# Kernel tuning notes

Measured on AMD Instinct MI355X. Metric: run time of the kernel, lower is better.

Reference implementation:

```python
import jax, jax.numpy as jnp
import numpy as np

N_NODES = 100000   # embedding table rows
FEAT = 512         # feat_dim F
BATCH = 8192       # seed nodes per batch
DEG = 32           # sampled neighbors per node (col 0 = self)
BN_EPS = 1e-5


def setup_inputs() -> dict:
    key = jax.random.key(0)
    ks = jax.random.split(key, 6)
    feat_table = jax.random.normal(ks[0], (N_NODES, FEAT), dtype=jnp.float32)
    W_gen = jax.random.normal(ks[1], (2 * FEAT, 2 * FEAT), dtype=jnp.float32) * 0.02
    weight1 = jax.random.normal(ks[2], (3 * FEAT, 3 * FEAT), dtype=jnp.float32) * 0.02
    gamma = jnp.ones((3 * FEAT,), dtype=jnp.float32)
    beta = jnp.zeros((3 * FEAT,), dtype=jnp.float32)
    nodes = jax.random.randint(ks[3], (BATCH,), 0, N_NODES, dtype=jnp.int32)
    neigh_idx = jax.random.randint(ks[4], (BATCH, DEG), 0, N_NODES, dtype=jnp.int32)
    neigh_idx = neigh_idx.at[:, 0].set(nodes)  # self node included, as in samp_neighs
    return {"feat_table": feat_table, "W_gen": W_gen, "weight1": weight1,
            "gamma": gamma, "beta": beta, "nodes": nodes, "neigh_idx": neigh_idx}


def _batchnorm_train(x, gamma, beta):
    # BatchNorm1d in training mode: biased batch statistics over axis 0
    mu = x.mean(axis=0)
    var = x.var(axis=0)
    return (x - mu) * jax.lax.rsqrt(var + BN_EPS) * gamma + beta


def _gen(x, W_gen):
    # generator module: raw = x @ W_gen, gen = relu(raw) (shape-preserving [B,2F])
    raw = x @ W_gen
    return jax.nn.relu(raw), raw


def reference(feat_table, W_gen, weight1, gamma, beta, nodes, neigh_idx):
    # self features: [B, F]
    self_feats = feat_table[nodes]
    # gather neighbor feats [B, K, F] and mean-pool (replaces dense mask.mm)
    neigh_feats = feat_table[neigh_idx]
    agg_feats = neigh_feats.mean(axis=1)                 # [B, F]
    cat_feats = jnp.concatenate([self_feats, agg_feats], axis=1)  # [B, 2F]
    gen_feats, raw_feats = _gen(cat_feats, W_gen)        # [B, 2F] each

    # environment aggregation: self node (column 0) removed from neighbor set
    env_agg_feats = neigh_feats[:, 1:, :].mean(axis=1)   # [B, F]
    env_cat = jnp.concatenate([jnp.zeros_like(self_feats), env_agg_feats], axis=1)
    env_gen_feats, env_raw_feats = _gen(env_cat, W_gen)

    # train_flag=True, rl_train_flag=False path
    feats = jnp.concatenate([agg_feats, gen_feats], axis=1)  # [B, 3F]
    to_feats = jax.nn.relu(_batchnorm_train(feats, gamma, beta) @ weight1)
    return (agg_feats, to_feats, gen_feats, raw_feats, env_gen_feats, env_raw_feats)
```

## Files before the change

kernel.cpp:

```cpp
#include <hip/hip_runtime.h>
#include <hip/hip_bf16.h>

typedef unsigned short u16;
typedef unsigned int u32;
typedef __attribute__((ext_vector_type(8))) short short8;
typedef __attribute__((ext_vector_type(4))) float f32x4;

#define BATCH 8192
#define FEAT 512
#define DEG 32
#define BM 128
#define BN 128
#define BK 32

__device__ __forceinline__ float b2f(u16 h){
  union { u32 u; float f; } x; x.u = ((u32)h) << 16; return x.f;
}
__device__ __forceinline__ u16 f2b(float f){
  __hip_bfloat16 h = __float2bfloat16(f);
  return *reinterpret_cast<u16*>(&h);
}
__device__ __forceinline__ u32 pack2(float lo, float hi){
  return (u32)f2b(lo) | (((u32)f2b(hi)) << 16);
}

__device__ __forceinline__ f32x4 mfma_bf16_16x16x32(short8 a, short8 b, f32x4 c){
  asm("v_mfma_f32_16x16x32_bf16 %0, %1, %2, %0" : "+v"(c) : "v"(a), "v"(b));
  return c;
}

__device__ __forceinline__ void gload16(const u16* g, u16* l){
  __builtin_amdgcn_global_load_lds(
      (const __attribute__((address_space(1))) u32*)(const void*)g,
      (__attribute__((address_space(3))) u32*)(void*)l, 16, 0, 0);
}

__global__ __launch_bounds__(256) void gather_agg(
    const float* __restrict__ feat, const int* __restrict__ nodes,
    const int* __restrict__ nidx, float* __restrict__ out_agg,
    u16* __restrict__ cat_bf, u16* __restrict__ env_bf)
{
  const int b = blockIdx.x;
  const int t = threadIdx.x;
  __shared__ int idx[DEG];
  __shared__ int self_node;
  if (t < DEG) idx[t] = nidx[b * DEG + t];
  if (t == 64) self_node = nodes[b];
  __syncthreads();
  const int f = t * 2;
  float s0 = 0.f, s1 = 0.f;
  #pragma unroll 8
  for (int k = 0; k < DEG; ++k){
    const float2 v = *(const float2*)(feat + (size_t)idx[k] * FEAT + f);
    s0 += v.x; s1 += v.y;
  }
  const float2 sv = *(const float2*)(feat + (size_t)self_node * FEAT + f);
  const float a0 = s0 * (1.f/32.f), a1 = s1 * (1.f/32.f);
  const float e0 = (s0 - sv.x) * (1.f/31.f), e1 = (s1 - sv.y) * (1.f/31.f);
  *(float2*)(out_agg + (size_t)b * FEAT + f) = make_float2(a0, a1);
  *(u32*)(cat_bf + (size_t)b * 1024 + f) = pack2(sv.x, sv.y);
  *(u32*)(cat_bf + (size_t)b * 1024 + FEAT + f) = pack2(a0, a1);
  *(u32*)(env_bf + (size_t)b * FEAT + f) = pack2(e0, e1);
}

__global__ __launch_bounds__(256) void transpose_f2b(
    const float* __restrict__ in, u16* __restrict__ out, int R, int C)
{
  __shared__ float tile[32][33];
  const int c0 = blockIdx.x * 32, r0 = blockIdx.y * 32;
  const int x = threadIdx.x, y = threadIdx.y;
  #pragma unroll
  for (int i = 0; i < 32; i += 8)
    tile[y + i][x] = in[(size_t)(r0 + y + i) * C + (c0 + x)];
  __syncthreads();
  #pragma unroll
  for (int i = 0; i < 32; i += 8)
    out[(size_t)(c0 + y + i) * R + (r0 + x)] = f2b(tile[x][y + i]);
}

template<bool WRITE_RAW>
__device__ __forceinline__ void gemm_body(
    const u16* __restrict__ A, int lda, const u16* __restrict__ BT, int ldb,
    int K, float* __restrict__ Craw, float* __restrict__ Crelu, int ldc,
    int m0, int n0, u16* As, u16* Bs)
{
  const int t = threadIdx.x;
  const int wave = t >> 6, lane = t & 63;
  const int wr = wave >> 1, wc = wave & 1;
  const int lm = lane & 15, quad = lane >> 4;

  const int sr = wave * 32 + (lane >> 2);
  const int sc = (lane & 3) * 8;

  f32x4 acc[4][4] = {};

  for (int k0 = 0; k0 < K; k0 += BK){
    gload16(A  + (size_t)(m0 + sr)      * lda + k0 + sc, As + sr * 32 + sc);
    gload16(A  + (size_t)(m0 + sr + 16) * lda + k0 + sc, As + (sr + 16) * 32 + sc);
    gload16(BT + (size_t)(n0 + sr)      * ldb + k0 + sc, Bs + sr * 32 + sc);
    gload16(BT + (size_t)(n0 + sr + 16) * ldb + k0 + sc, Bs + (sr + 16) * 32 + sc);
    __syncthreads();
    short8 af[4], bf[4];
    #pragma unroll
    for (int i = 0; i < 4; ++i)
      af[i] = *(const short8*)&As[(wr * 64 + i * 16 + lm) * 32 + quad * 8];
    #pragma unroll
    for (int j = 0; j < 4; ++j)
      bf[j] = *(const short8*)&Bs[(wc * 64 + j * 16 + lm) * 32 + quad * 8];
    #pragma unroll
    for (int i = 0; i < 4; ++i)
      #pragma unroll
      for (int j = 0; j < 4; ++j)
        acc[i][j] = mfma_bf16_16x16x32(af[i], bf[j], acc[i][j]);
    __syncthreads();
  }
  #pragma unroll
  for (int i = 0; i < 4; ++i){
    const int row = m0 + wr * 64 + i * 16 + quad * 4;
    #pragma unroll
    for (int j = 0; j < 4; ++j){
      const int col = n0 + wc * 64 + j * 16 + lm;
      #pragma unroll
      for (int r = 0; r < 4; ++r){
        const float v = acc[i][j][r];
        const size_t off = (size_t)(row + r) * ldc + col;
        if (WRITE_RAW) Craw[off] = v;
        Crelu[off] = fmaxf(v, 0.f);
      }
    }
  }
}

__global__ __launch_bounds__(256) void gemm12(
    const u16* __restrict__ catA, const u16* __restrict__ envA,
    const u16* __restrict__ wgT,
    float* __restrict__ raw, float* __restrict__ gen,
    float* __restrict__ envraw, float* __restrict__ envgen)
{
  __shared__ __align__(16) u16 As[BM * BK];
  __shared__ __align__(16) u16 Bs[BN * BK];
  const int z = blockIdx.z;
  const u16* A  = z ? envA : catA;
  const int lda = z ? 512 : 1024;
  const int K   = z ? 512 : 1024;
  const u16* BT = z ? wgT + 512 : wgT;
  float* Craw   = z ? envraw : raw;
  float* Crelu  = z ? envgen : gen;
  gemm_body<true>(A, lda, BT, 1024, K, Craw, Crelu, 1024,
                  blockIdx.y * BM, blockIdx.x * BN, As, Bs);
}

__global__ __launch_bounds__(256) void gemm3(
    const u16* __restrict__ bnA, const u16* __restrict__ w1T,
    float* __restrict__ to_out)
{
  __shared__ __align__(16) u16 As[BM * BK];
  __shared__ __align__(16) u16 Bs[BN * BK];
  gemm_body<false>(bnA, 1536, w1T, 1536, 1536, nullptr, to_out, 1536,
                   blockIdx.y * BM, blockIdx.x * BN, As, Bs);
}

__global__ __launch_bounds__(256) void zero_f32(float* __restrict__ p, int n){
  const int i = blockIdx.x * 256 + threadIdx.x;
  if (i < n) p[i] = 0.f;
}

__global__ __launch_bounds__(256) void bn_partial(
    const float* __restrict__ agg, const float* __restrict__ gen,
    float* __restrict__ sums)
{
  const int l = threadIdx.x & 63;
  const int ty = threadIdx.x >> 6;
  const int c = blockIdx.x * 64 + l;
  const int r0 = blockIdx.y * 1024;
  float s = 0.f, q = 0.f;
  if (c < 512){
    for (int r = r0 + ty; r < r0 + 1024; r += 4){
      const float x = agg[(size_t)r * 512 + c];
      s += x; q += x * x;
    }
  } else {
    for (int r = r0 + ty; r < r0 + 1024; r += 4){
      const float x = gen[(size_t)r * 1024 + (c - 512)];
      s += x; q += x * x;
    }
  }
  __shared__ float sh[2][4][64];
  sh[0][ty][l] = s; sh[1][ty][l] = q;
  __syncthreads();
  if (ty == 0){
    s = sh[0][0][l] + sh[0][1][l] + sh[0][2][l] + sh[0][3][l];
    q = sh[1][0][l] + sh[1][1][l] + sh[1][2][l] + sh[1][3][l];
    atomicAdd(&sums[c], s);
    atomicAdd(&sums[1536 + c], q);
  }
}

__global__ __launch_bounds__(256) void bn_finalize(
    const float* __restrict__ sums, const float* __restrict__ gamma,
    const float* __restrict__ beta, float* __restrict__ sArr, float* __restrict__ tArr)
{
  const int c = blockIdx.x * 256 + threadIdx.x;
  if (c >= 1536) return;
  const float mean = sums[c] * (1.f / 8192.f);
  const float var = sums[1536 + c] * (1.f / 8192.f) - mean * mean;
  const float rs = rsqrtf(var + 1e-5f);
  const float sc = gamma[c] * rs;
  sArr[c] = sc;
  tArr[c] = beta[c] - mean * sc;
}

__global__ __launch_bounds__(384) void prep_bnA(
    const float* __restrict__ agg, const float* __restrict__ gen,
    const float* __restrict__ sArr, const float* __restrict__ tArr,
    u16* __restrict__ bnA)
{
  const int m = blockIdx.x;
  const int t = threadIdx.x;
  const int c = t * 4;
  const float4 x = (c < 512)
      ? *(const float4*)(agg + (size_t)m * 512 + c)
      : *(const float4*)(gen + (size_t)m * 1024 + (c - 512));
  const float4 s4 = *(const float4*)(sArr + c);
  const float4 t4 = *(const float4*)(tArr + c);
  const u32 lo = pack2(fmaf(x.x, s4.x, t4.x), fmaf(x.y, s4.y, t4.y));
  const u32 hi = pack2(fmaf(x.z, s4.z, t4.z), fmaf(x.w, s4.w, t4.w));
  *(uint2*)(bnA + (size_t)m * 1536 + c) = make_uint2(lo, hi);
}

extern "C" void kernel_launch(void* const* d_in, const int* in_sizes, int n_in,
                              void* d_out, int out_size, void* d_ws, size_t ws_size,
                              hipStream_t stream)
{
  const float* feat  = (const float*)d_in[0];
  const float* Wgen  = (const float*)d_in[1];
  const float* W1    = (const float*)d_in[2];
  const float* gamma = (const float*)d_in[3];
  const float* beta  = (const float*)d_in[4];
  const int* nodes   = (const int*)d_in[5];
  const int* nidx    = (const int*)d_in[6];

  float* o = (float*)d_out;
  float* out_agg    = o;
  float* out_to     = o + 4194304;
  float* out_gen    = o + 16777216;
  float* out_raw    = o + 25165824;
  float* out_envgen = o + 33554432;
  float* out_envraw = o + 41943040;

  char* w = (char*)d_ws;
  float* sums = (float*)w;
  float* sArr = (float*)(w + 12288);
  float* tArr = (float*)(w + 18432);
  u16* wgT    = (u16*)(w + 32768);
  u16* w1T    = (u16*)(w + 2129920);
  u16* cat_bf = (u16*)(w + 6848512);
  u16* env_bf = (u16*)(w + 23625728);
  u16* bnA_bf = (u16*)(w + 6848512);

  gather_agg<<<BATCH, 256, 0, stream>>>(feat, nodes, nidx, out_agg, cat_bf, env_bf);
  transpose_f2b<<<dim3(32, 32), dim3(32, 8), 0, stream>>>(Wgen, wgT, 1024, 1024);
  transpose_f2b<<<dim3(48, 48), dim3(32, 8), 0, stream>>>(W1, w1T, 1536, 1536);

  gemm12<<<dim3(8, 64, 2), 256, 0, stream>>>(
      cat_bf, env_bf, wgT, out_raw, out_gen, out_envraw, out_envgen);

  zero_f32<<<12, 256, 0, stream>>>(sums, 3072);
  bn_partial<<<dim3(24, 8), 256, 0, stream>>>(out_agg, out_gen, sums);
  bn_finalize<<<6, 256, 0, stream>>>(sums, gamma, beta, sArr, tArr);
  prep_bnA<<<BATCH, 384, 0, stream>>>(out_agg, out_gen, sArr, tArr, bnA_bf);

  gemm3<<<dim3(12, 64), 256, 0, stream>>>(bnA_bf, w1T, out_to);
}
```

Baseline: 598.4 us.

## Vectorize gather, drop atomics and fuse BN finalize into normalize kernel

The gather kernel now handles two batch rows per block with float4 loads and takes the self row from neighbor column 0, so it no longer reads `nodes` or loads the self row a second time. The batch-norm statistics become per-row-block partials written with float4 stores instead of atomics. This removes the zero and finalize launches, and each prep_bnA block now reduces the 8 partials itself. The aim is fewer launches and wider memory accesses, at the cost of redundant finalize arithmetic in every prep block and reuse of the wgT workspace region for the partials after gemm12 has consumed it.

```diff
diff --git a/kernel.cpp b/kernel.cpp
--- a/kernel.cpp
+++ b/kernel.cpp
@@ -13,9 +13,6 @@
 #define BN 128
 #define BK 32
 
-__device__ __forceinline__ float b2f(u16 h){
-  union { u32 u; float f; } x; x.u = ((u32)h) << 16; return x.f;
-}
 __device__ __forceinline__ u16 f2b(float f){
   __hip_bfloat16 h = __float2bfloat16(f);
   return *reinterpret_cast<u16*>(&h);
@@ -36,31 +33,31 @@
 }
 
 __global__ __launch_bounds__(256) void gather_agg(
-    const float* __restrict__ feat, const int* __restrict__ nodes,
-    const int* __restrict__ nidx, float* __restrict__ out_agg,
-    u16* __restrict__ cat_bf, u16* __restrict__ env_bf)
-{
-  const int b = blockIdx.x;
+    const float* __restrict__ feat, const int* __restrict__ nidx,
+    float* __restrict__ out_agg, u16* __restrict__ cat_bf, u16* __restrict__ env_bf)
+{
   const int t = threadIdx.x;
-  __shared__ int idx[DEG];
-  __shared__ int self_node;
-  if (t < DEG) idx[t] = nidx[b * DEG + t];
-  if (t == 64) self_node = nodes[b];
+  const int half = t >> 7, tl = t & 127;
+  const int b = blockIdx.x * 2 + half;
+  __shared__ int idx[2][DEG];
+  if (t < 2 * DEG)
+    idx[t >> 5][t & 31] = nidx[(size_t)(blockIdx.x * 2 + (t >> 5)) * DEG + (t & 31)];
   __syncthreads();
-  const int f = t * 2;
-  float s0 = 0.f, s1 = 0.f;
+  const int f = tl * 4;
+  const float4 sv = *(const float4*)(feat + (size_t)idx[half][0] * FEAT + f);
+  float4 s = sv;
   #pragma unroll 8
-  for (int k = 0; k < DEG; ++k){
-    const float2 v = *(const float2*)(feat + (size_t)idx[k] * FEAT + f);
-    s0 += v.x; s1 += v.y;
-  }
-  const float2 sv = *(const float2*)(feat + (size_t)self_node * FEAT + f);
-  const float a0 = s0 * (1.f/32.f), a1 = s1 * (1.f/32.f);
-  const float e0 = (s0 - sv.x) * (1.f/31.f), e1 = (s1 - sv.y) * (1.f/31.f);
-  *(float2*)(out_agg + (size_t)b * FEAT + f) = make_float2(a0, a1);
-  *(u32*)(cat_bf + (size_t)b * 1024 + f) = pack2(sv.x, sv.y);
-  *(u32*)(cat_bf + (size_t)b * 1024 + FEAT + f) = pack2(a0, a1);
-  *(u32*)(env_bf + (size_t)b * FEAT + f) = pack2(e0, e1);
+  for (int k = 1; k < DEG; ++k){
+    const float4 v = *(const float4*)(feat + (size_t)idx[half][k] * FEAT + f);
+    s.x += v.x; s.y += v.y; s.z += v.z; s.w += v.w;
+  }
+  const float4 a = make_float4(s.x*(1.f/32.f), s.y*(1.f/32.f), s.z*(1.f/32.f), s.w*(1.f/32.f));
+  const float4 e = make_float4((s.x-sv.x)*(1.f/31.f), (s.y-sv.y)*(1.f/31.f),
+                               (s.z-sv.z)*(1.f/31.f), (s.w-sv.w)*(1.f/31.f));
+  *(float4*)(out_agg + (size_t)b * FEAT + f) = a;
+  *(uint2*)(cat_bf + (size_t)b * 1024 + f)        = make_uint2(pack2(sv.x, sv.y), pack2(sv.z, sv.w));
+  *(uint2*)(cat_bf + (size_t)b * 1024 + FEAT + f) = make_uint2(pack2(a.x, a.y), pack2(a.z, a.w));
+  *(uint2*)(env_bf + (size_t)b * FEAT + f)        = make_uint2(pack2(e.x, e.y), pack2(e.z, e.w));
 }
 
 __global__ __launch_bounds__(256) void transpose_f2b(
@@ -160,71 +157,76 @@
                    blockIdx.y * BM, blockIdx.x * BN, As, Bs);
 }
 
-__global__ __launch_bounds__(256) void zero_f32(float* __restrict__ p, int n){
-  const int i = blockIdx.x * 256 + threadIdx.x;
-  if (i < n) p[i] = 0.f;
-}
-
 __global__ __launch_bounds__(256) void bn_partial(
     const float* __restrict__ agg, const float* __restrict__ gen,
-    float* __restrict__ sums)
-{
-  const int l = threadIdx.x & 63;
-  const int ty = threadIdx.x >> 6;
-  const int c = blockIdx.x * 64 + l;
+    float* __restrict__ partials)
+{
+  const int tq = threadIdx.x & 63, ty = threadIdx.x >> 6;
+  const int c = blockIdx.x * 256 + tq * 4;
   const int r0 = blockIdx.y * 1024;
-  float s = 0.f, q = 0.f;
+  float4 s = make_float4(0.f,0.f,0.f,0.f), q = make_float4(0.f,0.f,0.f,0.f);
   if (c < 512){
     for (int r = r0 + ty; r < r0 + 1024; r += 4){
-      const float x = agg[(size_t)r * 512 + c];
-      s += x; q += x * x;
+      const float4 x = *(const float4*)(agg + (size_t)r * 512 + c);
+      s.x += x.x; s.y += x.y; s.z += x.z; s.w += x.w;
+      q.x += x.x*x.x; q.y += x.y*x.y; q.z += x.z*x.z; q.w += x.w*x.w;
     }
   } else {
     for (int r = r0 + ty; r < r0 + 1024; r += 4){
-      const float x = gen[(size_t)r * 1024 + (c - 512)];
-      s += x; q += x * x;
+      const float4 x = *(const float4*)(gen + (size_t)r * 1024 + (c - 512));
+      s.x += x.x; s.y += x.y; s.z += x.z; s.w += x.w;
+      q.x += x.x*x.x; q.y += x.y*x.y; q.z += x.z*x.z; q.w += x.w*x.w;
     }
   }
-  __shared__ float sh[2][4][64];
-  sh[0][ty][l] = s; sh[1][ty][l] = q;
+  __shared__ float4 sh[2][4][64];
+  sh[0][ty][tq] = s; sh[1][ty][tq] = q;
   __syncthreads();
   if (ty == 0){
-    s = sh[0][0][l] + sh[0][1][l] + sh[0][2][l] + sh[0][3][l];
-    q = sh[1][0][l] + sh[1][1][l] + sh[1][2][l] + sh[1][3][l];
-    atomicAdd(&sums[c], s);
-    atomicAdd(&sums[1536 + c], q);
-  }
-}
-
-__global__ __launch_bounds__(256) void bn_finalize(
-    const float* __restrict__ sums, const float* __restrict__ gamma,
-    const float* __restrict__ beta, float* __restrict__ sArr, float* __restrict__ tArr)
-{
-  const int c = blockIdx.x * 256 + threadIdx.x;
-  if (c >= 1536) return;
-  const float mean = sums[c] * (1.f / 8192.f);
-  const float var = sums[1536 + c] * (1.f / 8192.f) - mean * mean;
-  const float rs = rsqrtf(var + 1e-5f);
-  const float sc = gamma[c] * rs;
-  sArr[c] = sc;
-  tArr[c] = beta[c] - mean * sc;
+    float4 s0 = sh[0][0][tq], s1 = sh[0][1][tq], s2 = sh[0][2][tq], s3 = sh[0][3][tq];
+    float4 q0 = sh[1][0][tq], q1 = sh[1][1][tq], q2 = sh[1][2][tq], q3 = sh[1][3][tq];
+    const float4 S = make_float4(s0.x+s1.x+s2.x+s3.x, s0.y+s1.y+s2.y+s3.y,
+                                 s0.z+s1.z+s2.z+s3.z, s0.w+s1.w+s2.w+s3.w);
+    const float4 Q = make_float4(q0.x+q1.x+q2.x+q3.x, q0.y+q1.y+q2.y+q3.y,
+                                 q0.z+q1.z+q2.z+q3.z, q0.w+q1.w+q2.w+q3.w);
+    *(float4*)(partials + (size_t)blockIdx.y * 3072 + c)        = S;
+    *(float4*)(partials + (size_t)blockIdx.y * 3072 + 1536 + c) = Q;
+  }
 }
 
 __global__ __launch_bounds__(384) void prep_bnA(
     const float* __restrict__ agg, const float* __restrict__ gen,
-    const float* __restrict__ sArr, const float* __restrict__ tArr,
-    u16* __restrict__ bnA)
+    const float* __restrict__ partials, const float* __restrict__ gamma,
+    const float* __restrict__ beta, u16* __restrict__ bnA)
 {
   const int m = blockIdx.x;
   const int t = threadIdx.x;
   const int c = t * 4;
+  float4 s = make_float4(0.f,0.f,0.f,0.f), q = make_float4(0.f,0.f,0.f,0.f);
+  #pragma unroll
+  for (int k = 0; k < 8; ++k){
+    const float4 sk = *(const float4*)(partials + (size_t)k * 3072 + c);
+    const float4 qk = *(const float4*)(partials + (size_t)k * 3072 + 1536 + c);
+    s.x += sk.x; s.y += sk.y; s.z += sk.z; s.w += sk.w;
+    q.x += qk.x; q.y += qk.y; q.z += qk.z; q.w += qk.w;
+  }
+  const float4 g4 = *(const float4*)(gamma + c);
+  const float4 b4 = *(const float4*)(beta + c);
+  float sc[4], tc[4];
+  {
+    const float mean0 = s.x*(1.f/8192.f), var0 = q.x*(1.f/8192.f) - mean0*mean0;
+    const float mean1 = s.y*(1.f/8192.f), var1 = q.y*(1.f/8192.f) - mean1*mean1;
+    const float mean2 = s.z*(1.f/8192.f), var2 = q.z*(1.f/8192.f) - mean2*mean2;
+    const float mean3 = s.w*(1.f/8192.f), var3 = q.w*(1.f/8192.f) - mean3*mean3;
+    sc[0] = g4.x * rsqrtf(var0 + 1e-5f); tc[0] = b4.x - mean0 * sc[0];
+    sc[1] = g4.y * rsqrtf(var1 + 1e-5f); tc[1] = b4.y - mean1 * sc[1];
+    sc[2] = g4.z * rsqrtf(var2 + 1e-5f); tc[2] = b4.z - mean2 * sc[2];
+    sc[3] = g4.w * rsqrtf(var3 + 1e-5f); tc[3] = b4.w - mean3 * sc[3];
+  }
   const float4 x = (c < 512)
       ? *(const float4*)(agg + (size_t)m * 512 + c)
       : *(const float4*)(gen + (size_t)m * 1024 + (c - 512));
-  const float4 s4 = *(const float4*)(sArr + c);
-  const float4 t4 = *(const float4*)(tArr + c);
-  const u32 lo = pack2(fmaf(x.x, s4.x, t4.x), fmaf(x.y, s4.y, t4.y));
-  const u32 hi = pack2(fmaf(x.z, s4.z, t4.z), fmaf(x.w, s4.w, t4.w));
+  const u32 lo = pack2(fmaf(x.x, sc[0], tc[0]), fmaf(x.y, sc[1], tc[1]));
+  const u32 hi = pack2(fmaf(x.z, sc[2], tc[2]), fmaf(x.w, sc[3], tc[3]));
   *(uint2*)(bnA + (size_t)m * 1536 + c) = make_uint2(lo, hi);
 }
 
@@ -237,7 +239,6 @@
   const float* W1    = (const float*)d_in[2];
   const float* gamma = (const float*)d_in[3];
   const float* beta  = (const float*)d_in[4];
-  const int* nodes   = (const int*)d_in[5];
   const int* nidx    = (const int*)d_in[6];
 
   float* o = (float*)d_out;
@@ -249,26 +250,22 @@
   float* out_envraw = o + 41943040;
 
   char* w = (char*)d_ws;
-  float* sums = (float*)w;
-  float* sArr = (float*)(w + 12288);
-  float* tArr = (float*)(w + 18432);
   u16* wgT    = (u16*)(w + 32768);
+  float* partials = (float*)(w + 32768);
   u16* w1T    = (u16*)(w + 2129920);
   u16* cat_bf = (u16*)(w + 6848512);
   u16* env_bf = (u16*)(w + 23625728);
   u16* bnA_bf = (u16*)(w + 6848512);
 
-  gather_agg<<<BATCH, 256, 0, stream>>>(feat, nodes, nidx, out_agg, cat_bf, env_bf);
+  gather_agg<<<BATCH / 2, 256, 0, stream>>>(feat, nidx, out_agg, cat_bf, env_bf);
   transpose_f2b<<<dim3(32, 32), dim3(32, 8), 0, stream>>>(Wgen, wgT, 1024, 1024);
   transpose_f2b<<<dim3(48, 48), dim3(32, 8), 0, stream>>>(W1, w1T, 1536, 1536);
 
   gemm12<<<dim3(8, 64, 2), 256, 0, stream>>>(
       cat_bf, env_bf, wgT, out_raw, out_gen, out_envraw, out_envgen);
 
-  zero_f32<<<12, 256, 0, stream>>>(sums, 3072);
-  bn_partial<<<dim3(24, 8), 256, 0, stream>>>(out_agg, out_gen, sums);
-  bn_finalize<<<6, 256, 0, stream>>>(sums, gamma, beta, sArr, tArr);
-  prep_bnA<<<BATCH, 384, 0, stream>>>(out_agg, out_gen, sArr, tArr, bnA_bf);
+  bn_partial<<<dim3(6, 8), 256, 0, stream>>>(out_agg, out_gen, partials);
+  prep_bnA<<<BATCH, 384, 0, stream>>>(out_agg, out_gen, partials, gamma, beta, bnA_bf);
 
   gemm3<<<dim3(12, 64), 256, 0, stream>>>(bnA_bf, w1T, out_to);
 }
```

Result: slower. 629.1 us (+5.1%).
